# Performance work log

Measured on AMD Instinct MI355X. Metric: run time of the kernel, lower is better.

## Reference

```python
import jax, jax.numpy as jnp
import numpy as np

WS = 7           # window size
N = WS * WS      # tokens per window = 49
C = 128          # embed dim
H = 4            # heads
HD = C // H      # head dim = 32
NW = 64          # num windows (mask leading dim)
B = 4096         # total windows = outer_batch * NW


def _relative_indexes():
    ch = np.arange(WS)
    cw = np.arange(WS)
    coords = np.stack(np.meshgrid(ch, cw, indexing='ij')).reshape(2, -1)  # [2, N]
    rel = coords[:, :, None] - coords[:, None, :]                          # [2, N, N]
    rel = rel.transpose(1, 2, 0)
    rel[:, :, 0] += WS - 1
    rel[:, :, 1] += WS - 1
    rel[:, :, 0] *= 2 * WS - 1
    return jnp.asarray(rel.sum(-1), dtype=jnp.int32)                       # [N, N]


def setup_inputs() -> dict:
    key = jax.random.key(0)
    ks = jax.random.split(key, 10)
    s = 0.02
    return {
        'query': jax.random.normal(ks[0], (B, N, C), jnp.float32),
        'source': jax.random.normal(ks[1], (B, N, C), jnp.float32),
        'mask': jnp.zeros((NW, N, N), jnp.float32),
        'q_w': jax.random.normal(ks[2], (C, C), jnp.float32) * s,
        'q_b': jnp.zeros((C,), jnp.float32),
        'kv_w': jax.random.normal(ks[3], (C, 2 * C), jnp.float32) * s,
        'kv_b': jnp.zeros((2 * C,), jnp.float32),
        'proj_w': jax.random.normal(ks[4], (C, C), jnp.float32) * s,
        'proj_b': jnp.zeros((C,), jnp.float32),
        'bias_table': jax.random.normal(ks[5], ((2 * WS - 1) ** 2, H), jnp.float32) * s,
        'rel_idx': _relative_indexes(),
    }


def reference(query, source, mask, q_w, q_b, kv_w, kv_b, proj_w, proj_b, bias_table, rel_idx):
    scale = HD ** -0.5
    q = query @ q_w + q_b                       # [B, N, C]
    kv = source @ kv_w + kv_b                   # [B, N, 2C]
    k, v = kv[..., :C], kv[..., C:]
    # [B, N, H, HD] -> [B, H, N, HD]
    q = q.reshape(B, N, H, HD).transpose(0, 2, 1, 3) * scale
    k = k.reshape(B, N, H, HD).transpose(0, 2, 1, 3)
    v = v.reshape(B, N, H, HD).transpose(0, 2, 1, 3)
    attn = jnp.einsum('bhnd,bhmd->bhnm', q, k)  # [B, H, N, N]
    # gathered relative positional bias: [1, H, N, N]
    bias = bias_table[rel_idx.reshape(-1)].reshape(N, N, H).transpose(2, 0, 1)[None]
    attn = attn + bias
    # mask: [NW, N, N] broadcast over outer batch and heads
    attn = attn.reshape(-1, NW, H, N, N) + mask[None, :, None]
    attn = attn.reshape(B, H, N, N)
    attn = jax.nn.softmax(attn, axis=-1)
    x = jnp.einsum('bhnm,bhmd->bnhd', attn, v).reshape(B, N, C)
    return x @ proj_w + proj_b
```

## Files before the change

### kernel.cpp

```cpp
#include <hip/hip_runtime.h>

#define NN 49
#define CC 128
#define HH 4
#define NWIN 64
#define BB 4096
#define QSCALE 0.17677669529663687f

typedef __attribute__((ext_vector_type(8))) short bf16x8;
typedef __attribute__((ext_vector_type(4))) float f32x4;
typedef unsigned short u16;
typedef unsigned int u32;

__device__ __forceinline__ u16 f2b(float f) {
    u32 x = __float_as_uint(f);
    return (u16)((x + 0x7fffu + ((x >> 16) & 1u)) >> 16);
}
__device__ __forceinline__ float b2f(u16 u) { return __uint_as_float(((u32)u) << 16); }
__device__ __forceinline__ uint2 pack4(float a, float b, float c, float d) {
    uint2 r;
    r.x = (u32)f2b(a) | ((u32)f2b(b) << 16);
    r.y = (u32)f2b(c) | ((u32)f2b(d) << 16);
    return r;
}
__device__ __forceinline__ f32x4 mfma16(bf16x8 a, bf16x8 b, f32x4 c) {
    return __builtin_amdgcn_mfma_f32_16x16x32_bf16(a, b, c, 0, 0, 0);
}
__device__ __forceinline__ char* adr256(u16* base, int row, int byte) {
    return (char*)base + row * 256 + (byte ^ ((row & 7) << 4));
}
__device__ __forceinline__ char* adr128(u16* base, int row, int byte) {
    return (char*)base + row * 128 + (byte ^ ((row & 7) << 4));
}

__global__ void prep_cbt(const float* __restrict__ bias_table, const int* __restrict__ rel_idx,
                         const float* __restrict__ mask, u16* __restrict__ cbt) {
    int idx = blockIdx.x * blockDim.x + threadIdx.x;
    int m = idx & 63, i = (idx >> 6) & 63, h = (idx >> 12) & 3, wv = idx >> 14;
    if (wv >= NWIN) return;
    float v = -1e9f;
    if (m < NN && i < NN)
        v = bias_table[rel_idx[i * NN + m] * HH + h] + mask[(wv * NN + i) * NN + m];
    cbt[idx] = f2b(v);
}

__global__ void prep_w(const float* __restrict__ qw, const float* __restrict__ qb,
                       const float* __restrict__ kvw, const float* __restrict__ pjw,
                       u16* __restrict__ qwp, u16* __restrict__ kvwp,
                       u16* __restrict__ pjwp, float* __restrict__ qbs) {
    int idx = blockIdx.x * blockDim.x + threadIdx.x;
    if (idx < 16384) {
        int i = idx & 7, lane = (idx >> 3) & 63, kt = (idx >> 9) & 3, nt = idx >> 11;
        int k = 32 * kt + 8 * (lane >> 4) + i, n = 16 * nt + (lane & 15);
        qwp[idx] = f2b(qw[k * CC + n] * QSCALE);
    } else if (idx < 49152) {
        int j = idx - 16384;
        int i = j & 7, lane = (j >> 3) & 63, kt = (j >> 9) & 3, nt = j >> 11;
        int k = 32 * kt + 8 * (lane >> 4) + i, n = 16 * nt + (lane & 15);
        kvwp[j] = f2b(kvw[k * 2 * CC + n]);
    } else if (idx < 65536) {
        int j = idx - 49152;
        int i = j & 7, lane = (j >> 3) & 63, kt = (j >> 9) & 3, nt = j >> 11;
        int k = 32 * kt + 8 * (lane >> 4) + i, n = 16 * nt + (lane & 15);
        pjwp[j] = f2b(pjw[k * CC + n]);
    } else if (idx < 65664) {
        int j = idx - 65536;
        qbs[j] = qb[j] * QSCALE;
    }
}

__global__ __launch_bounds__(256, 3)
void wmha_main(const float* __restrict__ query, const float* __restrict__ source,
               const u16* __restrict__ qwp, const u16* __restrict__ kvwp,
               const u16* __restrict__ pjwp, const float* __restrict__ qbs,
               const float* __restrict__ kv_b, const float* __restrict__ proj_b,
               const u16* __restrict__ cbt, float* __restrict__ out) {
    __shared__ u16 lds[24576];
    u16* R0 = lds;
    u16* R1 = lds + 8192;
    u16* R2 = lds + 16384;
    const int t = threadIdx.x;
    const int b = blockIdx.x;
    const int w = t >> 6, lane = t & 63;
    const int lq = lane & 15, qd = lane >> 4;

    {
        const int row = t >> 2, qu = t & 3;
        const size_t gbase = (size_t)b * NN * CC + row * CC + qu * 32;
        #pragma unroll
        for (int j = 0; j < 4; ++j) {
            bf16x8 vq = {0,0,0,0,0,0,0,0}, vs = {0,0,0,0,0,0,0,0};
            if (row < NN) {
                const float4* q4 = (const float4*)(query + gbase) + 2 * j;
                const float4* s4 = (const float4*)(source + gbase) + 2 * j;
                float4 a0 = q4[0], a1 = q4[1], c0 = s4[0], c1 = s4[1];
                vq[0]=(short)f2b(a0.x); vq[1]=(short)f2b(a0.y); vq[2]=(short)f2b(a0.z); vq[3]=(short)f2b(a0.w);
                vq[4]=(short)f2b(a1.x); vq[5]=(short)f2b(a1.y); vq[6]=(short)f2b(a1.z); vq[7]=(short)f2b(a1.w);
                vs[0]=(short)f2b(c0.x); vs[1]=(short)f2b(c0.y); vs[2]=(short)f2b(c0.z); vs[3]=(short)f2b(c0.w);
                vs[4]=(short)f2b(c1.x); vs[5]=(short)f2b(c1.y); vs[6]=(short)f2b(c1.z); vs[7]=(short)f2b(c1.w);
            }
            *(bf16x8*)adr256(R0, row, qu * 64 + 16 * j) = vq;
            *(bf16x8*)adr256(R2, row, qu * 64 + 16 * j) = vs;
        }
    }
    bf16x8 bwq[2][4];
    #pragma unroll
    for (int n2 = 0; n2 < 2; ++n2)
        #pragma unroll
        for (int kt = 0; kt < 4; ++kt)
            bwq[n2][kt] = *(const bf16x8*)(qwp + (((w + 4 * n2) * 4 + kt) * 64 + lane) * 8);
    __syncthreads();

    {
        f32x4 acc[4][2] = {};
        __builtin_amdgcn_s_setprio(1);
        #pragma unroll
        for (int mt = 0; mt < 4; ++mt) {
            bf16x8 a[4];
            #pragma unroll
            for (int kt = 0; kt < 4; ++kt)
                a[kt] = *(const bf16x8*)adr256(R0, mt * 16 + lq, kt * 64 + qd * 16);
            #pragma unroll
            for (int n2 = 0; n2 < 2; ++n2)
                #pragma unroll
                for (int kt = 0; kt < 4; ++kt)
                    acc[mt][n2] = mfma16(a[kt], bwq[n2][kt], acc[mt][n2]);
        }
        __builtin_amdgcn_s_setprio(0);
        #pragma unroll
        for (int n2 = 0; n2 < 2; ++n2) {
            const int col = 16 * (w + 4 * n2) + lq;
            const float bias = qbs[col];
            #pragma unroll
            for (int mt = 0; mt < 4; ++mt)
                #pragma unroll
                for (int r = 0; r < 4; ++r) {
                    const int row = mt * 16 + qd * 4 + r;
                    *(u16*)adr256(R1, row, 2 * col) = f2b(acc[mt][n2][r] + bias);
                }
        }
    }
    __syncthreads();

    {
        bf16x8 bw[2][4];
        #pragma unroll
        for (int n2 = 0; n2 < 2; ++n2)
            #pragma unroll
            for (int kt = 0; kt < 4; ++kt)
                bw[n2][kt] = *(const bf16x8*)(kvwp + (((w + 4 * n2) * 4 + kt) * 64 + lane) * 8);
        f32x4 acc[4][2] = {};
        __builtin_amdgcn_s_setprio(1);
        #pragma unroll
        for (int mt = 0; mt < 4; ++mt) {
            bf16x8 a[4];
            #pragma unroll
            for (int kt = 0; kt < 4; ++kt)
                a[kt] = *(const bf16x8*)adr256(R2, mt * 16 + lq, kt * 64 + qd * 16);
            #pragma unroll
            for (int n2 = 0; n2 < 2; ++n2)
                #pragma unroll
                for (int kt = 0; kt < 4; ++kt)
                    acc[mt][n2] = mfma16(a[kt], bw[n2][kt], acc[mt][n2]);
        }
        __builtin_amdgcn_s_setprio(0);
        #pragma unroll
        for (int n2 = 0; n2 < 2; ++n2) {
            const int col = 16 * (w + 4 * n2) + lq;
            const float bias = kv_b[col];
            #pragma unroll
            for (int mt = 0; mt < 4; ++mt)
                #pragma unroll
                for (int r = 0; r < 4; ++r) {
                    const int row = mt * 16 + qd * 4 + r;
                    *(u16*)adr256(R0, row, 2 * col) = f2b(acc[mt][n2][r] + bias);
                }
        }
    }

    {
        bf16x8 bw[2][4];
        #pragma unroll
        for (int n2 = 0; n2 < 2; ++n2)
            #pragma unroll
            for (int kt = 0; kt < 4; ++kt)
                bw[n2][kt] = *(const bf16x8*)(kvwp + (((w + 8 + 4 * n2) * 4 + kt) * 64 + lane) * 8);
        f32x4 acc[4][2] = {};
        __builtin_amdgcn_s_setprio(1);
        #pragma unroll
        for (int mt = 0; mt < 4; ++mt) {
            bf16x8 a[4];
            #pragma unroll
            for (int kt = 0; kt < 4; ++kt)
                a[kt] = *(const bf16x8*)adr256(R2, mt * 16 + lq, kt * 64 + qd * 16);
            #pragma unroll
            for (int n2 = 0; n2 < 2; ++n2)
                #pragma unroll
                for (int kt = 0; kt < 4; ++kt)
                    acc[mt][n2] = mfma16(a[kt], bw[n2][kt], acc[mt][n2]);
        }
        __builtin_amdgcn_s_setprio(0);
        __syncthreads();
        #pragma unroll
        for (int n2 = 0; n2 < 2; ++n2) {
            const int dim = 16 * w + 64 * n2 + lq;
            const float bias = kv_b[CC + dim];
            #pragma unroll
            for (int mt = 0; mt < 4; ++mt) {
                uint2 pk = pack4(acc[mt][n2][0] + bias, acc[mt][n2][1] + bias,
                                 acc[mt][n2][2] + bias, acc[mt][n2][3] + bias);
                *(uint2*)adr128(R2, dim, 2 * (mt * 16 + qd * 4)) = pk;
            }
        }
    }

    const int h = w;
    f32x4 s[4][4];
    {
        bf16x8 kf[4];
        #pragma unroll
        for (int a = 0; a < 4; ++a)
            kf[a] = *(const bf16x8*)adr256(R0, a * 16 + lq, h * 64 + qd * 16);
        __builtin_amdgcn_s_setprio(1);
        #pragma unroll
        for (int bq = 0; bq < 4; ++bq) {
            bf16x8 qf = *(const bf16x8*)adr256(R1, bq * 16 + lq, h * 64 + qd * 16);
            f32x4 z = {0.f, 0.f, 0.f, 0.f};
            #pragma unroll
            for (int a = 0; a < 4; ++a)
                s[bq][a] = mfma16(kf[a], qf, z);
        }
        __builtin_amdgcn_s_setprio(0);
    }
    __syncthreads();

    {
        bf16x8 vf[2][2];
        #pragma unroll
        for (int dt = 0; dt < 2; ++dt)
            #pragma unroll
            for (int kt = 0; kt < 2; ++kt)
                vf[dt][kt] = *(const bf16x8*)adr128(R2, h * 32 + dt * 16 + lq, kt * 64 + qd * 16);
        u16* pb = R0 + w * 1024;
        const u16* cbb = cbt + ((size_t)((b & (NWIN - 1)) * HH + h) << 12);
        #pragma unroll
        for (int bq = 0; bq < 4; ++bq) {
            uint2 cb2[4];
            #pragma unroll
            for (int a = 0; a < 4; ++a)
                cb2[a] = *(const uint2*)(cbb + (bq * 16 + lq) * 64 + a * 16 + qd * 4);
            #pragma unroll
            for (int a = 0; a < 4; ++a) {
                s[bq][a][0] += b2f((u16)(cb2[a].x & 0xffffu));
                s[bq][a][1] += b2f((u16)(cb2[a].x >> 16));
                s[bq][a][2] += b2f((u16)(cb2[a].y & 0xffffu));
                s[bq][a][3] += b2f((u16)(cb2[a].y >> 16));
            }
            float m0 = s[bq][0][0];
            #pragma unroll
            for (int a = 0; a < 4; ++a)
                #pragma unroll
                for (int r = 0; r < 4; ++r) m0 = fmaxf(m0, s[bq][a][r]);
            m0 = fmaxf(m0, __shfl_xor(m0, 16));
            m0 = fmaxf(m0, __shfl_xor(m0, 32));
            uint2 pk[4];
            float sm = 0.f;
            #pragma unroll
            for (int a = 0; a < 4; ++a) {
                float p0 = __expf(s[bq][a][0] - m0), p1 = __expf(s[bq][a][1] - m0);
                float p2 = __expf(s[bq][a][2] - m0), p3 = __expf(s[bq][a][3] - m0);
                pk[a] = pack4(p0, p1, p2, p3);
                sm += b2f((u16)pk[a].x) + b2f((u16)(pk[a].x >> 16))
                    + b2f((u16)pk[a].y) + b2f((u16)(pk[a].y >> 16));
            }
            sm += __shfl_xor(sm, 16);
            sm += __shfl_xor(sm, 32);
            const float inv = 1.f / sm;
            #pragma unroll
            for (int a = 0; a < 4; ++a)
                *(uint2*)adr128(pb, lq, 32 * a + 8 * qd) = pk[a];
            asm volatile("s_waitcnt lgkmcnt(0)" ::: "memory");
            __builtin_amdgcn_sched_barrier(0);
            f32x4 o[2] = {{0.f,0.f,0.f,0.f},{0.f,0.f,0.f,0.f}};
            __builtin_amdgcn_s_setprio(1);
            #pragma unroll
            for (int kt = 0; kt < 2; ++kt) {
                bf16x8 pf = *(const bf16x8*)adr128(pb, lq, 64 * kt + 16 * qd);
                #pragma unroll
                for (int dt = 0; dt < 2; ++dt)
                    o[dt] = mfma16(vf[dt][kt], pf, o[dt]);
            }
            __builtin_amdgcn_s_setprio(0);
            __builtin_amdgcn_sched_barrier(0);
            #pragma unroll
            for (int dt = 0; dt < 2; ++dt) {
                uint2 px = pack4(o[dt][0] * inv, o[dt][1] * inv,
                                 o[dt][2] * inv, o[dt][3] * inv);
                *(uint2*)adr256(R1, bq * 16 + lq, 64 * h + 32 * dt + 8 * qd) = px;
            }
        }
    }

    {
        bf16x8 bw[2][4];
        #pragma unroll
        for (int n2 = 0; n2 < 2; ++n2)
            #pragma unroll
            for (int kt = 0; kt < 4; ++kt)
                bw[n2][kt] = *(const bf16x8*)(pjwp + (((w + 4 * n2) * 4 + kt) * 64 + lane) * 8);
        __syncthreads();
        f32x4 acc[4][2] = {};
        __builtin_amdgcn_s_setprio(1);
        #pragma unroll
        for (int mt = 0; mt < 4; ++mt) {
            bf16x8 a[4];
            #pragma unroll
            for (int kt = 0; kt < 4; ++kt)
                a[kt] = *(const bf16x8*)adr256(R1, mt * 16 + lq, kt * 64 + qd * 16);
            #pragma unroll
            for (int n2 = 0; n2 < 2; ++n2)
                #pragma unroll
                for (int kt = 0; kt < 4; ++kt)
                    acc[mt][n2] = mfma16(a[kt], bw[n2][kt], acc[mt][n2]);
        }
        __builtin_amdgcn_s_setprio(0);
        float* outb = out + (size_t)b * NN * CC;
        #pragma unroll
        for (int n2 = 0; n2 < 2; ++n2) {
            const int col = 16 * (w + 4 * n2) + lq;
            const float bias = proj_b[col];
            #pragma unroll
            for (int mt = 0; mt < 4; ++mt)
                #pragma unroll
                for (int r = 0; r < 4; ++r) {
                    const int row = mt * 16 + qd * 4 + r;
                    if (row < NN) outb[row * CC + col] = acc[mt][n2][r] + bias;
                }
        }
    }
}

extern "C" void kernel_launch(void* const* d_in, const int* in_sizes, int n_in,
                              void* d_out, int out_size, void* d_ws, size_t ws_size,
                              hipStream_t stream) {
    const float* query      = (const float*)d_in[0];
    const float* source     = (const float*)d_in[1];
    const float* mask       = (const float*)d_in[2];
    const float* q_w        = (const float*)d_in[3];
    const float* q_b        = (const float*)d_in[4];
    const float* kv_w       = (const float*)d_in[5];
    const float* kv_b       = (const float*)d_in[6];
    const float* proj_w     = (const float*)d_in[7];
    const float* proj_b     = (const float*)d_in[8];
    const float* bias_table = (const float*)d_in[9];
    const int*   rel_idx    = (const int*)d_in[10];
    float* out = (float*)d_out;

    u16* cbt   = (u16*)d_ws;
    u16* qwp   = cbt + 1048576;
    u16* kvwp  = qwp + 16384;
    u16* pjwp  = kvwp + 32768;
    float* qbs = (float*)(pjwp + 16384);

    prep_cbt<<<4096, 256, 0, stream>>>(bias_table, rel_idx, mask, cbt);
    prep_w<<<257, 256, 0, stream>>>(q_w, q_b, kv_w, proj_w, qwp, kvwp, pjwp, qbs);
    wmha_main<<<BB, 256, 0, stream>>>(query, source, qwp, kvwp, pjwp, qbs,
                                      kv_b, proj_b, cbt, out);
}
```

Before: 125.3 us.

## Use packed bf16 converts, transposed MFMA epilogues, and paired softmax rows

Swaps the manual bf16 rounding for the hardware v_cvt_pk_bf16_f32 instruction. Swaps MFMA operand order in the Q, K and projection GEMMs so each lane holds four consecutive columns, which allows vectorized uint2 LDS stores and float4 global output stores instead of scalar ones. Prefetches the combined bias/mask tile into registers before the barrier and processes two query row-blocks per softmax/PV step, using double P buffers to issue more MFMAs between waits. It also moves setprio inside the loops and sums fp32 probabilities instead of the rounded bf16 ones, which slightly changes the numerics and raises register pressure.

```diff
diff --git a/kernel.cpp b/kernel.cpp
--- a/kernel.cpp
+++ b/kernel.cpp
@@ -1,4 +1,5 @@
 #include <hip/hip_runtime.h>
+#include <hip/hip_bf16.h>
 
 #define NN 49
 #define CC 128
@@ -12,15 +13,22 @@
 typedef unsigned short u16;
 typedef unsigned int u32;
 
+union U8 { u32 u[4]; bf16x8 v; };
+
 __device__ __forceinline__ u16 f2b(float f) {
-    u32 x = __float_as_uint(f);
-    return (u16)((x + 0x7fffu + ((x >> 16) & 1u)) >> 16);
+    __hip_bfloat16 h = __float2bfloat16(f);
+    return __builtin_bit_cast(u16, h);
 }
 __device__ __forceinline__ float b2f(u16 u) { return __uint_as_float(((u32)u) << 16); }
+__device__ __forceinline__ u32 cvtpk(float lo, float hi) {
+    u32 r;
+    asm("v_cvt_pk_bf16_f32 %0, %1, %2" : "=v"(r) : "v"(lo), "v"(hi));
+    return r;
+}
 __device__ __forceinline__ uint2 pack4(float a, float b, float c, float d) {
     uint2 r;
-    r.x = (u32)f2b(a) | ((u32)f2b(b) << 16);
-    r.y = (u32)f2b(c) | ((u32)f2b(d) << 16);
+    r.x = cvtpk(a, b);
+    r.y = cvtpk(c, d);
     return r;
 }
 __device__ __forceinline__ f32x4 mfma16(bf16x8 a, bf16x8 b, f32x4 c) {
@@ -83,24 +91,28 @@
     const int b = blockIdx.x;
     const int w = t >> 6, lane = t & 63;
     const int lq = lane & 15, qd = lane >> 4;
+    const int h = w;
 
     {
         const int row = t >> 2, qu = t & 3;
         const size_t gbase = (size_t)b * NN * CC + row * CC + qu * 32;
         #pragma unroll
         for (int j = 0; j < 4; ++j) {
-            bf16x8 vq = {0,0,0,0,0,0,0,0}, vs = {0,0,0,0,0,0,0,0};
+            U8 vq, vs;
             if (row < NN) {
                 const float4* q4 = (const float4*)(query + gbase) + 2 * j;
                 const float4* s4 = (const float4*)(source + gbase) + 2 * j;
                 float4 a0 = q4[0], a1 = q4[1], c0 = s4[0], c1 = s4[1];
-                vq[0]=(short)f2b(a0.x); vq[1]=(short)f2b(a0.y); vq[2]=(short)f2b(a0.z); vq[3]=(short)f2b(a0.w);
-                vq[4]=(short)f2b(a1.x); vq[5]=(short)f2b(a1.y); vq[6]=(short)f2b(a1.z); vq[7]=(short)f2b(a1.w);
-                vs[0]=(short)f2b(c0.x); vs[1]=(short)f2b(c0.y); vs[2]=(short)f2b(c0.z); vs[3]=(short)f2b(c0.w);
-                vs[4]=(short)f2b(c1.x); vs[5]=(short)f2b(c1.y); vs[6]=(short)f2b(c1.z); vs[7]=(short)f2b(c1.w);
-            }
-            *(bf16x8*)adr256(R0, row, qu * 64 + 16 * j) = vq;
-            *(bf16x8*)adr256(R2, row, qu * 64 + 16 * j) = vs;
+                vq.u[0] = cvtpk(a0.x, a0.y); vq.u[1] = cvtpk(a0.z, a0.w);
+                vq.u[2] = cvtpk(a1.x, a1.y); vq.u[3] = cvtpk(a1.z, a1.w);
+                vs.u[0] = cvtpk(c0.x, c0.y); vs.u[1] = cvtpk(c0.z, c0.w);
+                vs.u[2] = cvtpk(c1.x, c1.y); vs.u[3] = cvtpk(c1.z, c1.w);
+            } else {
+                vq.u[0] = vq.u[1] = vq.u[2] = vq.u[3] = 0;
+                vs.u[0] = vs.u[1] = vs.u[2] = vs.u[3] = 0;
+            }
+            *(bf16x8*)adr256(R0, row, qu * 64 + 16 * j) = vq.v;
+            *(bf16x8*)adr256(R2, row, qu * 64 + 16 * j) = vs.v;
         }
     }
     bf16x8 bwq[2][4];
@@ -113,124 +125,139 @@
 
     {
         f32x4 acc[4][2] = {};
-        __builtin_amdgcn_s_setprio(1);
         #pragma unroll
         for (int mt = 0; mt < 4; ++mt) {
             bf16x8 a[4];
             #pragma unroll
             for (int kt = 0; kt < 4; ++kt)
                 a[kt] = *(const bf16x8*)adr256(R0, mt * 16 + lq, kt * 64 + qd * 16);
+            __builtin_amdgcn_s_setprio(1);
             #pragma unroll
             for (int n2 = 0; n2 < 2; ++n2)
                 #pragma unroll
                 for (int kt = 0; kt < 4; ++kt)
-                    acc[mt][n2] = mfma16(a[kt], bwq[n2][kt], acc[mt][n2]);
-        }
-        __builtin_amdgcn_s_setprio(0);
+                    acc[mt][n2] = mfma16(bwq[n2][kt], a[kt], acc[mt][n2]);
+            __builtin_amdgcn_s_setprio(0);
+        }
         #pragma unroll
         for (int n2 = 0; n2 < 2; ++n2) {
-            const int col = 16 * (w + 4 * n2) + lq;
-            const float bias = qbs[col];
-            #pragma unroll
-            for (int mt = 0; mt < 4; ++mt)
-                #pragma unroll
-                for (int r = 0; r < 4; ++r) {
-                    const int row = mt * 16 + qd * 4 + r;
-                    *(u16*)adr256(R1, row, 2 * col) = f2b(acc[mt][n2][r] + bias);
-                }
+            const int cb0 = 16 * (w + 4 * n2) + 4 * qd;
+            const float4 bia = *(const float4*)(qbs + cb0);
+            #pragma unroll
+            for (int mt = 0; mt < 4; ++mt) {
+                const int tok = mt * 16 + lq;
+                uint2 pk = pack4(acc[mt][n2][0] + bia.x, acc[mt][n2][1] + bia.y,
+                                 acc[mt][n2][2] + bia.z, acc[mt][n2][3] + bia.w);
+                *(uint2*)adr256(R1, tok, 2 * cb0) = pk;
+            }
         }
     }
     __syncthreads();
 
     {
-        bf16x8 bw[2][4];
+        bf16x8 bwk[2][4];
         #pragma unroll
         for (int n2 = 0; n2 < 2; ++n2)
             #pragma unroll
             for (int kt = 0; kt < 4; ++kt)
-                bw[n2][kt] = *(const bf16x8*)(kvwp + (((w + 4 * n2) * 4 + kt) * 64 + lane) * 8);
+                bwk[n2][kt] = *(const bf16x8*)(kvwp + (((w + 4 * n2) * 4 + kt) * 64 + lane) * 8);
         f32x4 acc[4][2] = {};
-        __builtin_amdgcn_s_setprio(1);
         #pragma unroll
         for (int mt = 0; mt < 4; ++mt) {
             bf16x8 a[4];
             #pragma unroll
             for (int kt = 0; kt < 4; ++kt)
                 a[kt] = *(const bf16x8*)adr256(R2, mt * 16 + lq, kt * 64 + qd * 16);
+            __builtin_amdgcn_s_setprio(1);
             #pragma unroll
             for (int n2 = 0; n2 < 2; ++n2)
                 #pragma unroll
                 for (int kt = 0; kt < 4; ++kt)
-                    acc[mt][n2] = mfma16(a[kt], bw[n2][kt], acc[mt][n2]);
-        }
-        __builtin_amdgcn_s_setprio(0);
+                    acc[mt][n2] = mfma16(bwk[n2][kt], a[kt], acc[mt][n2]);
+            __builtin_amdgcn_s_setprio(0);
+        }
         #pragma unroll
         for (int n2 = 0; n2 < 2; ++n2) {
-            const int col = 16 * (w + 4 * n2) + lq;
-            const float bias = kv_b[col];
-            #pragma unroll
-            for (int mt = 0; mt < 4; ++mt)
-                #pragma unroll
-                for (int r = 0; r < 4; ++r) {
-                    const int row = mt * 16 + qd * 4 + r;
-                    *(u16*)adr256(R0, row, 2 * col) = f2b(acc[mt][n2][r] + bias);
-                }
-        }
-    }
-
-    {
-        bf16x8 bw[2][4];
+            const int cb0 = 16 * (w + 4 * n2) + 4 * qd;
+            const float4 bia = *(const float4*)(kv_b + cb0);
+            #pragma unroll
+            for (int mt = 0; mt < 4; ++mt) {
+                const int tok = mt * 16 + lq;
+                uint2 pk = pack4(acc[mt][n2][0] + bia.x, acc[mt][n2][1] + bia.y,
+                                 acc[mt][n2][2] + bia.z, acc[mt][n2][3] + bia.w);
+                *(uint2*)adr256(R0, tok, 2 * cb0) = pk;
+            }
+        }
+    }
+
+    {
+        bf16x8 bwv[2][4];
         #pragma unroll
         for (int n2 = 0; n2 < 2; ++n2)
             #pragma unroll
             for (int kt = 0; kt < 4; ++kt)
-                bw[n2][kt] = *(const bf16x8*)(kvwp + (((w + 8 + 4 * n2) * 4 + kt) * 64 + lane) * 8);
+                bwv[n2][kt] = *(const bf16x8*)(kvwp + (((8 + w + 4 * n2) * 4 + kt) * 64 + lane) * 8);
         f32x4 acc[4][2] = {};
-        __builtin_amdgcn_s_setprio(1);
         #pragma unroll
         for (int mt = 0; mt < 4; ++mt) {
             bf16x8 a[4];
             #pragma unroll
             for (int kt = 0; kt < 4; ++kt)
                 a[kt] = *(const bf16x8*)adr256(R2, mt * 16 + lq, kt * 64 + qd * 16);
+            __builtin_amdgcn_s_setprio(1);
             #pragma unroll
             for (int n2 = 0; n2 < 2; ++n2)
                 #pragma unroll
                 for (int kt = 0; kt < 4; ++kt)
-                    acc[mt][n2] = mfma16(a[kt], bw[n2][kt], acc[mt][n2]);
-        }
-        __builtin_amdgcn_s_setprio(0);
+                    acc[mt][n2] = mfma16(a[kt], bwv[n2][kt], acc[mt][n2]);
+            __builtin_amdgcn_s_setprio(0);
+        }
+        uint2 pkv[2][4];
+        #pragma unroll
+        for (int n2 = 0; n2 < 2; ++n2) {
+            const float bias = kv_b[CC + 16 * (w + 4 * n2) + lq];
+            #pragma unroll
+            for (int mt = 0; mt < 4; ++mt)
+                pkv[n2][mt] = pack4(acc[mt][n2][0] + bias, acc[mt][n2][1] + bias,
+                                    acc[mt][n2][2] + bias, acc[mt][n2][3] + bias);
+        }
         __syncthreads();
         #pragma unroll
         for (int n2 = 0; n2 < 2; ++n2) {
-            const int dim = 16 * w + 64 * n2 + lq;
-            const float bias = kv_b[CC + dim];
-            #pragma unroll
-            for (int mt = 0; mt < 4; ++mt) {
-                uint2 pk = pack4(acc[mt][n2][0] + bias, acc[mt][n2][1] + bias,
-                                 acc[mt][n2][2] + bias, acc[mt][n2][3] + bias);
-                *(uint2*)adr128(R2, dim, 2 * (mt * 16 + qd * 4)) = pk;
-            }
-        }
-    }
-
-    const int h = w;
+            const int dim = 16 * (w + 4 * n2) + lq;
+            #pragma unroll
+            for (int mt = 0; mt < 4; ++mt)
+                *(uint2*)adr128(R2, dim, 2 * (mt * 16 + qd * 4)) = pkv[n2][mt];
+        }
+    }
+
     f32x4 s[4][4];
     {
-        bf16x8 kf[4];
+        bf16x8 kf[4], qf[4];
         #pragma unroll
         for (int a = 0; a < 4; ++a)
             kf[a] = *(const bf16x8*)adr256(R0, a * 16 + lq, h * 64 + qd * 16);
+        #pragma unroll
+        for (int bq = 0; bq < 4; ++bq)
+            qf[bq] = *(const bf16x8*)adr256(R1, bq * 16 + lq, h * 64 + qd * 16);
         __builtin_amdgcn_s_setprio(1);
         #pragma unroll
         for (int bq = 0; bq < 4; ++bq) {
-            bf16x8 qf = *(const bf16x8*)adr256(R1, bq * 16 + lq, h * 64 + qd * 16);
             f32x4 z = {0.f, 0.f, 0.f, 0.f};
             #pragma unroll
             for (int a = 0; a < 4; ++a)
-                s[bq][a] = mfma16(kf[a], qf, z);
+                s[bq][a] = mfma16(kf[a], qf[bq], z);
         }
         __builtin_amdgcn_s_setprio(0);
+    }
+    uint2 cbr[4][4];
+    {
+        const u16* cbb = cbt + ((size_t)((b & (NWIN - 1)) * HH + h) << 12);
+        #pragma unroll
+        for (int bq = 0; bq < 4; ++bq)
+            #pragma unroll
+            for (int a = 0; a < 4; ++a)
+                cbr[bq][a] = *(const uint2*)(cbb + (bq * 16 + lq) * 64 + a * 16 + qd * 4);
     }
     __syncthreads();
 
@@ -241,63 +268,70 @@
             #pragma unroll
             for (int kt = 0; kt < 2; ++kt)
                 vf[dt][kt] = *(const bf16x8*)adr128(R2, h * 32 + dt * 16 + lq, kt * 64 + qd * 16);
-        u16* pb = R0 + w * 1024;
-        const u16* cbb = cbt + ((size_t)((b & (NWIN - 1)) * HH + h) << 12);
-        #pragma unroll
-        for (int bq = 0; bq < 4; ++bq) {
-            uint2 cb2[4];
-            #pragma unroll
-            for (int a = 0; a < 4; ++a)
-                cb2[a] = *(const uint2*)(cbb + (bq * 16 + lq) * 64 + a * 16 + qd * 4);
-            #pragma unroll
-            for (int a = 0; a < 4; ++a) {
-                s[bq][a][0] += b2f((u16)(cb2[a].x & 0xffffu));
-                s[bq][a][1] += b2f((u16)(cb2[a].x >> 16));
-                s[bq][a][2] += b2f((u16)(cb2[a].y & 0xffffu));
-                s[bq][a][3] += b2f((u16)(cb2[a].y >> 16));
-            }
-            float m0 = s[bq][0][0];
-            #pragma unroll
-            for (int a = 0; a < 4; ++a)
-                #pragma unroll
-                for (int r = 0; r < 4; ++r) m0 = fmaxf(m0, s[bq][a][r]);
-            m0 = fmaxf(m0, __shfl_xor(m0, 16));
-            m0 = fmaxf(m0, __shfl_xor(m0, 32));
-            uint2 pk[4];
-            float sm = 0.f;
-            #pragma unroll
-            for (int a = 0; a < 4; ++a) {
-                float p0 = __expf(s[bq][a][0] - m0), p1 = __expf(s[bq][a][1] - m0);
-                float p2 = __expf(s[bq][a][2] - m0), p3 = __expf(s[bq][a][3] - m0);
-                pk[a] = pack4(p0, p1, p2, p3);
-                sm += b2f((u16)pk[a].x) + b2f((u16)(pk[a].x >> 16))
-                    + b2f((u16)pk[a].y) + b2f((u16)(pk[a].y >> 16));
-            }
-            sm += __shfl_xor(sm, 16);
-            sm += __shfl_xor(sm, 32);
-            const float inv = 1.f / sm;
-            #pragma unroll
-            for (int a = 0; a < 4; ++a)
-                *(uint2*)adr128(pb, lq, 32 * a + 8 * qd) = pk[a];
+        u16* pb0 = R0 + w * 2048;
+        u16* pb1 = pb0 + 1024;
+        #pragma unroll
+        for (int p = 0; p < 2; ++p) {
+            float inv[2];
+            #pragma unroll
+            for (int i = 0; i < 2; ++i) {
+                const int bq = 2 * p + i;
+                #pragma unroll
+                for (int a = 0; a < 4; ++a) {
+                    s[bq][a][0] += b2f((u16)(cbr[bq][a].x & 0xffffu));
+                    s[bq][a][1] += b2f((u16)(cbr[bq][a].x >> 16));
+                    s[bq][a][2] += b2f((u16)(cbr[bq][a].y & 0xffffu));
+                    s[bq][a][3] += b2f((u16)(cbr[bq][a].y >> 16));
+                }
+                float m0 = s[bq][0][0];
+                #pragma unroll
+                for (int a = 0; a < 4; ++a)
+                    #pragma unroll
+                    for (int r = 0; r < 4; ++r) m0 = fmaxf(m0, s[bq][a][r]);
+                m0 = fmaxf(m0, __shfl_xor(m0, 16));
+                m0 = fmaxf(m0, __shfl_xor(m0, 32));
+                uint2 pk[4];
+                float sm = 0.f;
+                #pragma unroll
+                for (int a = 0; a < 4; ++a) {
+                    float p0 = __expf(s[bq][a][0] - m0), p1 = __expf(s[bq][a][1] - m0);
+                    float p2 = __expf(s[bq][a][2] - m0), p3 = __expf(s[bq][a][3] - m0);
+                    pk[a].x = cvtpk(p0, p1);
+                    pk[a].y = cvtpk(p2, p3);
+                    sm += (p0 + p1) + (p2 + p3);
+                }
+                sm += __shfl_xor(sm, 16);
+                sm += __shfl_xor(sm, 32);
+                inv[i] = 1.f / sm;
+                u16* pb = i ? pb1 : pb0;
+                #pragma unroll
+                for (int a = 0; a < 4; ++a)
+                    *(uint2*)adr128(pb, lq, 32 * a + 8 * qd) = pk[a];
+            }
             asm volatile("s_waitcnt lgkmcnt(0)" ::: "memory");
             __builtin_amdgcn_sched_barrier(0);
-            f32x4 o[2] = {{0.f,0.f,0.f,0.f},{0.f,0.f,0.f,0.f}};
+            f32x4 o[2][2] = {};
             __builtin_amdgcn_s_setprio(1);
             #pragma unroll
             for (int kt = 0; kt < 2; ++kt) {
-                bf16x8 pf = *(const bf16x8*)adr128(pb, lq, 64 * kt + 16 * qd);
-                #pragma unroll
-                for (int dt = 0; dt < 2; ++dt)
-                    o[dt] = mfma16(vf[dt][kt], pf, o[dt]);
+                bf16x8 pf0 = *(const bf16x8*)adr128(pb0, lq, 64 * kt + 16 * qd);
+                bf16x8 pf1 = *(const bf16x8*)adr128(pb1, lq, 64 * kt + 16 * qd);
+                #pragma unroll
+                for (int dt = 0; dt < 2; ++dt) {
+                    o[0][dt] = mfma16(vf[dt][kt], pf0, o[0][dt]);
+                    o[1][dt] = mfma16(vf[dt][kt], pf1, o[1][dt]);
+                }
             }
             __builtin_amdgcn_s_setprio(0);
             __builtin_amdgcn_sched_barrier(0);
             #pragma unroll
-            for (int dt = 0; dt < 2; ++dt) {
-                uint2 px = pack4(o[dt][0] * inv, o[dt][1] * inv,
-                                 o[dt][2] * inv, o[dt][3] * inv);
-                *(uint2*)adr256(R1, bq * 16 + lq, 64 * h + 32 * dt + 8 * qd) = px;
-            }
+            for (int i = 0; i < 2; ++i)
+                #pragma unroll
+                for (int dt = 0; dt < 2; ++dt) {
+                    uint2 px = pack4(o[i][dt][0] * inv[i], o[i][dt][1] * inv[i],
+                                     o[i][dt][2] * inv[i], o[i][dt][3] * inv[i]);
+                    *(uint2*)adr256(R1, (2 * p + i) * 16 + lq, 64 * h + 32 * dt + 8 * qd) = px;
+                }
         }
     }
 
@@ -310,32 +344,37 @@
                 bw[n2][kt] = *(const bf16x8*)(pjwp + (((w + 4 * n2) * 4 + kt) * 64 + lane) * 8);
         __syncthreads();
         f32x4 acc[4][2] = {};
-        __builtin_amdgcn_s_setprio(1);
         #pragma unroll
         for (int mt = 0; mt < 4; ++mt) {
             bf16x8 a[4];
             #pragma unroll
             for (int kt = 0; kt < 4; ++kt)
                 a[kt] = *(const bf16x8*)adr256(R1, mt * 16 + lq, kt * 64 + qd * 16);
+            __builtin_amdgcn_s_setprio(1);
             #pragma unroll
             for (int n2 = 0; n2 < 2; ++n2)
                 #pragma unroll
                 for (int kt = 0; kt < 4; ++kt)
-                    acc[mt][n2] = mfma16(a[kt], bw[n2][kt], acc[mt][n2]);
-        }
-        __builtin_amdgcn_s_setprio(0);
+                    acc[mt][n2] = mfma16(bw[n2][kt], a[kt], acc[mt][n2]);
+            __builtin_amdgcn_s_setprio(0);
+        }
         float* outb = out + (size_t)b * NN * CC;
         #pragma unroll
         for (int n2 = 0; n2 < 2; ++n2) {
-            const int col = 16 * (w + 4 * n2) + lq;
-            const float bias = proj_b[col];
-            #pragma unroll
-            for (int mt = 0; mt < 4; ++mt)
-                #pragma unroll
-                for (int r = 0; r < 4; ++r) {
-                    const int row = mt * 16 + qd * 4 + r;
-                    if (row < NN) outb[row * CC + col] = acc[mt][n2][r] + bias;
+            const int cb0 = 16 * (w + 4 * n2) + 4 * qd;
+            const float4 bia = *(const float4*)(proj_b + cb0);
+            #pragma unroll
+            for (int mt = 0; mt < 4; ++mt) {
+                const int tok = mt * 16 + lq;
+                if (tok < NN) {
+                    float4 vst;
+                    vst.x = acc[mt][n2][0] + bia.x;
+                    vst.y = acc[mt][n2][1] + bia.y;
+                    vst.z = acc[mt][n2][2] + bia.z;
+                    vst.w = acc[mt][n2][3] + bia.w;
+                    *(float4*)(outb + tok * CC + cb0) = vst;
                 }
+            }
         }
     }
 }
```

Measured after the change: 128.6 us. +2.6%, slower.
